# Optimization experiments

Hardware: AMD Instinct MI355X
Metric: run time of the kernel (lower is better)

The kernel has to match this reference:

```python
import jax, jax.numpy as jnp
import numpy as np

B, T, C, H = 4, 2048, 1024, 16
HD = C // H


def setup_inputs() -> dict:
    key = jax.random.key(0)
    kx, kq, ko = jax.random.split(key, 3)
    x = jax.random.normal(kx, (B, T, C), dtype=jnp.float32)
    # torch nn.Linear weight layout: [out_features, in_features]
    wqkv = jax.random.normal(kq, (3 * C, C), dtype=jnp.float32) * (1.0 / np.sqrt(C))
    wo = jax.random.normal(ko, (C, C), dtype=jnp.float32) * (1.0 / np.sqrt(C))
    return {"x": x, "wqkv": wqkv, "wo": wo}


def reference(x, wqkv, wo):
    Bn, Tn, Cn = x.shape
    # fused QKV projection: x @ wqkv.T -> [B, T, 3C]
    qkv = jnp.einsum('btc,dc->btd', x, wqkv)
    qkv = qkv.reshape(Bn, Tn, 3, H, HD)
    q = qkv[:, :, 0].transpose(0, 2, 1, 3)  # [B, H, T, hd]
    k = qkv[:, :, 1].transpose(0, 2, 1, 3)
    v = qkv[:, :, 2].transpose(0, 2, 1, 3)
    scale = 1.0 / np.sqrt(HD).astype(np.float32)
    scores = jnp.einsum('bhqd,bhkd->bhqk', q, k) * scale  # [B, H, T, T]
    causal = jnp.tril(jnp.ones((Tn, Tn), dtype=bool))
    scores = jnp.where(causal, scores, jnp.finfo(scores.dtype).min)
    attn = jax.nn.softmax(scores, axis=-1)
    y = jnp.einsum('bhqk,bhkd->bhqd', attn, v)  # [B, H, T, hd]
    y = y.transpose(0, 2, 1, 3).reshape(Bn, Tn, Cn)
    return jnp.einsum('btc,dc->btd', y, wo)
```

## Files before the change

### kernel.cpp

```cpp
#include <hip/hip_runtime.h>
#include <hip/hip_bf16.h>
#include <stdint.h>


typedef __attribute__((ext_vector_type(8))) short short8;
typedef __attribute__((ext_vector_type(4))) float f32x4;
typedef __attribute__((ext_vector_type(4))) float float4v;
typedef __attribute__((ext_vector_type(4))) unsigned short ushort4v;
typedef __attribute__((ext_vector_type(4))) unsigned int u32x4;

#define AS1 __attribute__((address_space(1)))
#define AS3 __attribute__((address_space(3)))

#if __has_builtin(__builtin_amdgcn_exp2f)
#define EXP2(x) __builtin_amdgcn_exp2f(x)
#else
#define EXP2(x) __expf((x) * 0.69314718f)
#endif

static __device__ __forceinline__ void gload_lds16(const void* g, void* l) {
  __builtin_amdgcn_global_load_lds((const AS1 void*)g, (AS3 void*)l, 16, 0, 0);
}

__global__ void k_detect(const unsigned int* __restrict__ x, int* __restrict__ flag) {
  __shared__ int sm[256];
  int c = 0;
  for (int i = 0; i < 8; ++i) {
    unsigned int v = x[threadIdx.x * 8 + i];
    unsigned int e = (v >> 7) & 0xffu;
    if (e >= 110u && e <= 140u) c++;
  }
  sm[threadIdx.x] = c;
  __syncthreads();
  if (threadIdx.x == 0) {
    int t = 0;
    for (int i = 0; i < 256; ++i) t += sm[i];
    *flag = (t > 1024) ? 1 : 0;
  }
}

__global__ void k_convert3(const void* __restrict__ xs, const void* __restrict__ wqs,
                           const void* __restrict__ wos, unsigned short* __restrict__ out,
                           const int* __restrict__ flag) {
  const int f = *flag;
  const int stride = gridDim.x * blockDim.x;
  for (int v = blockIdx.x * blockDim.x + threadIdx.x; v < 3145728; v += stride) {
    const int i = v * 4;
    const void* src; int j;
    if (i < 8388608)        { src = xs;  j = i; }
    else if (i < 11534336)  { src = wqs; j = i - 8388608; }
    else                    { src = wos; j = i - 11534336; }
    ushort4v r;
    if (f) {
      r = *(const ushort4v*)((const unsigned short*)src + j);
    } else {
      float4v fv = *(const float4v*)((const float*)src + j);
#pragma unroll
      for (int e = 0; e < 4; e++) {
        __hip_bfloat16 h = __float2bfloat16(fv[e]);
        r[e] = *(unsigned short*)&h;
      }
    }
    *(ushort4v*)(out + i) = r;
  }
}

__global__ __launch_bounds__(512) void k_gemm_qkv(
    const __hip_bfloat16* __restrict__ X, const __hip_bfloat16* __restrict__ W,
    __hip_bfloat16* __restrict__ qo, __hip_bfloat16* __restrict__ ko,
    __hip_bfloat16* __restrict__ vto) {
  __shared__ __align__(16) __hip_bfloat16 As[3][128 * 32];
  __shared__ __align__(16) __hip_bfloat16 Bs[3][128 * 32];
  const int tid = threadIdx.x;
  const int lane = tid & 63;
  const int wid = tid >> 6;
  const int wr = wid & 3, wc = wid >> 2;
  const int lr = lane & 15, lk = lane >> 4;
  const int m0 = blockIdx.x * 128;
  const int n0 = blockIdx.y * 128;
  const int sw = (lr >> 1) & 3;

  const int row = tid >> 2;
  const int ce = ((tid & 3) ^ ((row >> 1) & 3)) * 8;
  const int dst = (tid & ~63) * 8;

  const f32x4 fzero = {0.f, 0.f, 0.f, 0.f};
  f32x4 acc[2][4];
#pragma unroll
  for (int i = 0; i < 2; i++)
#pragma unroll
    for (int j = 0; j < 4; j++) acc[i][j] = fzero;

#define QKV_STAGE(buf, kt2)                                                        \
  {                                                                                \
    const int kk = (kt2) * 32;                                                     \
    gload_lds16(X + (size_t)(m0 + row) * 1024 + kk + ce, (void*)(As[buf] + dst));  \
    gload_lds16(W + (size_t)(n0 + row) * 1024 + kk + ce, (void*)(Bs[buf] + dst));  \
  }

  QKV_STAGE(0, 0)
  QKV_STAGE(1, 1)

  int cur = 0;
  for (int kt = 0; kt < 32; ++kt) {
    if (kt + 1 < 32) { asm volatile("s_waitcnt vmcnt(2)" ::: "memory"); }
    else             { asm volatile("s_waitcnt vmcnt(0)" ::: "memory"); }
    __builtin_amdgcn_s_barrier();
    __builtin_amdgcn_sched_barrier(0);

    short8 a[2], b[4];
#pragma unroll
    for (int i = 0; i < 2; i++) a[i] = *(const short8*)(As[cur] + (wr * 32 + i * 16 + lr) * 32 + ((lk ^ sw) * 8));
#pragma unroll
    for (int i = 0; i < 4; i++) b[i] = *(const short8*)(Bs[cur] + (wc * 64 + i * 16 + lr) * 32 + ((lk ^ sw) * 8));
#pragma unroll
    for (int mf = 0; mf < 2; mf++)
#pragma unroll
      for (int nf = 0; nf < 4; nf++)
        acc[mf][nf] = __builtin_amdgcn_mfma_f32_16x16x32_bf16(a[mf], b[nf], acc[mf][nf], 0, 0, 0);

    if (kt + 2 < 32) {
      int tb = cur + 2; if (tb >= 3) tb -= 3;
      QKV_STAGE(tb, kt + 2)
    }
    cur = (cur + 1 == 3) ? 0 : cur + 1;
  }
#undef QKV_STAGE

#pragma unroll
  for (int mf = 0; mf < 2; mf++)
#pragma unroll
    for (int nf = 0; nf < 4; nf++)
#pragma unroll
      for (int r = 0; r < 4; r++) {
        const int orow = m0 + wr * 32 + mf * 16 + lk * 4 + r;
        const int col = n0 + wc * 64 + nf * 16 + lr;
        const int s = col >> 10;
        const int rem = col & 1023;
        const int h = rem >> 6, hd = rem & 63;
        const int bb = orow >> 11, t = orow & 2047;
        const size_t bh = (size_t)(bb * 16 + h);
        if (s == 0) {
          qo[(bh * 2048 + t) * 64 + hd] = __float2bfloat16(acc[mf][nf][r] * 0.18033688f);
        } else if (s == 1) {
          ko[(bh * 2048 + t) * 64 + hd] = __float2bfloat16(acc[mf][nf][r]);
        } else {
          vto[(bh * 64 + hd) * 2048 + t] = __float2bfloat16(acc[mf][nf][r]);
        }
      }
}

__global__ __launch_bounds__(512) void k_attn(
    const __hip_bfloat16* __restrict__ Q, const __hip_bfloat16* __restrict__ K,
    const __hip_bfloat16* __restrict__ VT, __hip_bfloat16* __restrict__ Y) {
  __shared__ __align__(16) char smem[49152];
  char* smc = smem;
  const int tid = threadIdx.x, lane = tid & 63, wid = tid >> 6;
  const int lr = lane & 15, lk = lane >> 4;

  const int bid = blockIdx.x;
  const int bh = bid & 63;
  const int p = bid >> 6;
  const int e = p & 3;
  const int x = (p < 4) ? p : 7 - e;
  const int q0 = x * 256;
  const int qb = q0 + wid * 32;
  const size_t base = (size_t)bh * 2048 * 64;

  const int srow = tid >> 3;
  const int fs = (srow & 7) ^ ((2 * (srow >> 3)) & 7);
  const int scol = ((tid & 7) ^ fs) * 8;
  const __hip_bfloat16* kg = K + base + scol;
  const __hip_bfloat16* vg = VT + base + (size_t)srow * 2048 + scol;
  const int ldst = (tid & ~63) * 16;

  int koff[4][2], voff[4][2], kla[4];
#pragma unroll
  for (int a = 0; a < 4; a++) {
    const int ra = (lr >> 2) * 8 + (a & 1) * 4 + (lr & 3) + (a >> 1) * 32;
    const int fr = (ra & 7) ^ ((2 * (ra >> 3)) & 7);
    kla[a] = lk * 8 + (a & 1) * 4 + (a >> 1) * 32;
#pragma unroll
    for (int ks = 0; ks < 2; ks++)
      koff[a][ks] = ra * 128 + (((ks * 4 + lk) ^ fr) * 16);
  }
#pragma unroll
  for (int df = 0; df < 4; df++) {
    const int rv = df * 16 + lr;
    const int fv = (rv & 7) ^ ((2 * (rv >> 3)) & 7);
#pragma unroll
    for (int ks = 0; ks < 2; ks++)
      voff[df][ks] = rv * 128 + (((ks * 4 + lk) ^ fv) * 16);
  }

  short8 qf[2][2];
#pragma unroll
  for (int qg = 0; qg < 2; qg++)
#pragma unroll
    for (int ks = 0; ks < 2; ks++)
      qf[qg][ks] = *(const short8*)(Q + base + (size_t)(qb + qg * 16 + lr) * 64 + ks * 32 + lk * 8);

  const f32x4 fzero = {0.f, 0.f, 0.f, 0.f};
  f32x4 ot[2][4];
  float mrow[2] = {-1e30f, -1e30f}, lrow[2] = {0.f, 0.f};
#pragma unroll
  for (int qg = 0; qg < 2; qg++)
#pragma unroll
    for (int df = 0; df < 4; df++) ot[qg][df] = fzero;

  const int nkv = x * 4 + 4;
  gload_lds16(kg + (size_t)srow * 64, (void*)(smc + ldst));
  gload_lds16(vg, (void*)(smc + 24576 + ldst));
  gload_lds16(kg + (size_t)(64 + srow) * 64, (void*)(smc + 8192 + ldst));
  gload_lds16(vg + 64, (void*)(smc + 24576 + 8192 + ldst));

  int cur = 0;
  for (int kt = 0; kt < nkv; ++kt) {
    const int k0 = kt * 64;
    if (kt + 1 < nkv) { asm volatile("s_waitcnt vmcnt(2)" ::: "memory"); }
    else              { asm volatile("s_waitcnt vmcnt(0)" ::: "memory"); }
    __builtin_amdgcn_s_barrier();
    __builtin_amdgcn_sched_barrier(0);

    if (k0 <= qb + 31) {
      const char* kbuf = smc + cur * 8192;
      const char* vbuf = smc + 24576 + cur * 8192;

      f32x4 s[2][4];
#pragma unroll
      for (int qg = 0; qg < 2; qg++)
#pragma unroll
        for (int a = 0; a < 4; a++) s[qg][a] = fzero;

      __builtin_amdgcn_s_setprio(1);
#pragma unroll
      for (int ks = 0; ks < 2; ks++)
#pragma unroll
        for (int a = 0; a < 4; a++) {
          const short8 kb = *(const short8*)(kbuf + koff[a][ks]);
          s[0][a] = __builtin_amdgcn_mfma_f32_16x16x32_bf16(kb, qf[0][ks], s[0][a], 0, 0, 0);
          s[1][a] = __builtin_amdgcn_mfma_f32_16x16x32_bf16(kb, qf[1][ks], s[1][a], 0, 0, 0);
        }
      __builtin_amdgcn_s_setprio(0);

      const bool needmask = (k0 + 63 > qb);
      short8 pb[2][2];

#pragma unroll
      for (int qg = 0; qg < 2; qg++) {
        const int qq = qb + qg * 16 + lr;
        if (needmask) {
#pragma unroll
          for (int a = 0; a < 4; a++)
#pragma unroll
            for (int r = 0; r < 4; r++)
              if (k0 + kla[a] + r > qq) s[qg][a][r] = -1e30f;
        }
        f32x4 m4;
#pragma unroll
        for (int r = 0; r < 4; r++)
          m4[r] = fmaxf(fmaxf(s[qg][0][r], s[qg][1][r]), fmaxf(s[qg][2][r], s[qg][3][r]));
        float mx = fmaxf(fmaxf(m4[0], m4[1]), fmaxf(m4[2], m4[3]));
        mx = fmaxf(mx, __shfl_xor(mx, 16, 64));
        mx = fmaxf(mx, __shfl_xor(mx, 32, 64));
        const float mold = mrow[qg];
        float m;
        if (__all(mx - mold <= 8.f)) {
          m = mold;
        } else {
          m = fmaxf(mold, mx);
          const float alpha = EXP2(mold - m);
          lrow[qg] *= alpha;
          mrow[qg] = m;
#pragma unroll
          for (int df = 0; df < 4; df++) ot[qg][df] *= alpha;
        }
        float rs = 0.f;
#pragma unroll
        for (int a = 0; a < 4; a++)
#pragma unroll
          for (int r = 0; r < 4; r++) {
            const float pv = EXP2(s[qg][a][r] - m);
            s[qg][a][r] = pv;
            rs += pv;
          }
        lrow[qg] += rs;
#pragma unroll
        for (int ksP = 0; ksP < 2; ksP++) {
          short8 w;
#pragma unroll
          for (int ee = 0; ee < 4; ee++) {
            __hip_bfloat16 h0 = __float2bfloat16(s[qg][2 * ksP][ee]);
            __hip_bfloat16 h1 = __float2bfloat16(s[qg][2 * ksP + 1][ee]);
            w[ee] = *(short*)&h0;
            w[4 + ee] = *(short*)&h1;
          }
          pb[qg][ksP] = w;
        }
      }

      __builtin_amdgcn_s_setprio(1);
#pragma unroll
      for (int ks = 0; ks < 2; ks++)
#pragma unroll
        for (int df = 0; df < 4; df++) {
          const short8 vb = *(const short8*)(vbuf + voff[df][ks]);
          ot[0][df] = __builtin_amdgcn_mfma_f32_16x16x32_bf16(vb, pb[0][ks], ot[0][df], 0, 0, 0);
          ot[1][df] = __builtin_amdgcn_mfma_f32_16x16x32_bf16(vb, pb[1][ks], ot[1][df], 0, 0, 0);
        }
      __builtin_amdgcn_s_setprio(0);
    }

    if (kt + 2 < nkv) {
      const int kn = (kt + 2) * 64;
      int tb = cur + 2; if (tb >= 3) tb -= 3;
      gload_lds16(kg + (size_t)(kn + srow) * 64, (void*)(smc + tb * 8192 + ldst));
      gload_lds16(vg + kn, (void*)(smc + 24576 + tb * 8192 + ldst));
    }
    cur = (cur + 1 == 3) ? 0 : cur + 1;
  }

  __syncthreads();
  unsigned int* Os = (unsigned int*)smc;
#pragma unroll
  for (int qg = 0; qg < 2; qg++) {
    float ls = lrow[qg];
    ls += __shfl_xor(ls, 16, 64);
    ls += __shfl_xor(ls, 32, 64);
    const float inv = 1.f / ls;
    const int qlocal = wid * 32 + qg * 16 + lr;
    const int sw = (lr & 7) << 2;
#pragma unroll
    for (int df = 0; df < 4; df++)
#pragma unroll
      for (int e2 = 0; e2 < 2; e2++) {
        __hip_bfloat16 h0 = __float2bfloat16(ot[qg][df][2 * e2] * inv);
        __hip_bfloat16 h1 = __float2bfloat16(ot[qg][df][2 * e2 + 1] * inv);
        const unsigned int w = (unsigned int)*(unsigned short*)&h0 |
                               ((unsigned int)*(unsigned short*)&h1 << 16);
        Os[qlocal * 32 + ((df * 8 + lk * 2 + e2) ^ sw)] = w;
      }
  }
  __syncthreads();
  {
    const int qrow = tid >> 1, half = tid & 1, q7 = qrow & 7;
    const int b = bh >> 4, h = bh & 15;
    unsigned int* Yu = (unsigned int*)Y;
    const size_t rowbase = ((size_t)b * 2048 + q0 + qrow) * 512 + h * 32;
#pragma unroll
    for (int g = 0; g < 4; g++) {
      const int cg = half * 4 + g;
      const u32x4 v = *(const u32x4*)(smc + qrow * 128 + ((cg ^ q7) * 16));
      *(u32x4*)(Yu + rowbase + cg * 4) = v;
    }
  }
}

__global__ __launch_bounds__(512) void k_gemm_out(
    const __hip_bfloat16* __restrict__ X, const __hip_bfloat16* __restrict__ W,
    void* __restrict__ out, const int* __restrict__ flag) {
  __shared__ __align__(16) __hip_bfloat16 As[3][128 * 32];
  __shared__ __align__(16) __hip_bfloat16 Bs[3][128 * 32];
  const int tid = threadIdx.x;
  const int lane = tid & 63;
  const int wid = tid >> 6;
  const int wr = wid & 3, wc = wid >> 2;
  const int lr = lane & 15, lk = lane >> 4;
  const int m0 = blockIdx.x * 128;
  const int n0 = blockIdx.y * 128;
  const int sw = (lr >> 1) & 3;

  const int row = tid >> 2;
  const int ce = ((tid & 3) ^ ((row >> 1) & 3)) * 8;
  const int dst = (tid & ~63) * 8;

  const f32x4 fzero = {0.f, 0.f, 0.f, 0.f};
  f32x4 acc[2][4];
#pragma unroll
  for (int i = 0; i < 2; i++)
#pragma unroll
    for (int j = 0; j < 4; j++) acc[i][j] = fzero;

#define OUT_STAGE(buf, kt2)                                                        \
  {                                                                                \
    const int kk = (kt2) * 32;                                                     \
    gload_lds16(X + (size_t)(m0 + row) * 1024 + kk + ce, (void*)(As[buf] + dst));  \
    gload_lds16(W + (size_t)(n0 + row) * 1024 + kk + ce, (void*)(Bs[buf] + dst));  \
  }

  OUT_STAGE(0, 0)
  OUT_STAGE(1, 1)

  int cur = 0;
  for (int kt = 0; kt < 32; ++kt) {
    if (kt + 1 < 32) { asm volatile("s_waitcnt vmcnt(2)" ::: "memory"); }
    else             { asm volatile("s_waitcnt vmcnt(0)" ::: "memory"); }
    __builtin_amdgcn_s_barrier();
    __builtin_amdgcn_sched_barrier(0);

    short8 a[2], b[4];
#pragma unroll
    for (int i = 0; i < 2; i++) a[i] = *(const short8*)(As[cur] + (wr * 32 + i * 16 + lr) * 32 + ((lk ^ sw) * 8));
#pragma unroll
    for (int i = 0; i < 4; i++) b[i] = *(const short8*)(Bs[cur] + (wc * 64 + i * 16 + lr) * 32 + ((lk ^ sw) * 8));
#pragma unroll
    for (int mf = 0; mf < 2; mf++)
#pragma unroll
      for (int nf = 0; nf < 4; nf++)
        acc[mf][nf] = __builtin_amdgcn_mfma_f32_16x16x32_bf16(a[mf], b[nf], acc[mf][nf], 0, 0, 0);

    if (kt + 2 < 32) {
      int tb = cur + 2; if (tb >= 3) tb -= 3;
      OUT_STAGE(tb, kt + 2)
    }
    cur = (cur + 1 == 3) ? 0 : cur + 1;
  }
#undef OUT_STAGE

  const int f = *flag;
#pragma unroll
  for (int mf = 0; mf < 2; mf++)
#pragma unroll
    for (int nf = 0; nf < 4; nf++)
#pragma unroll
      for (int r = 0; r < 4; r++) {
        const int orow = m0 + wr * 32 + mf * 16 + lk * 4 + r;
        const int col = n0 + wc * 64 + nf * 16 + lr;
        const size_t oi = (size_t)orow * 1024 + col;
        if (f) ((__hip_bfloat16*)out)[oi] = __float2bfloat16(acc[mf][nf][r]);
        else   ((float*)out)[oi] = acc[mf][nf][r];
      }
}

extern "C" void kernel_launch(void* const* d_in, const int* in_sizes, int n_in,
                              void* d_out, int out_size, void* d_ws, size_t ws_size,
                              hipStream_t stream) {
  const void* x = d_in[0];
  const void* wqkv = d_in[1];
  const void* wo = d_in[2];

  char* ws = (char*)d_ws;
  int* flag = (int*)ws;
  __hip_bfloat16* xb    = (__hip_bfloat16*)(ws + 256);
  __hip_bfloat16* wqkvb = xb + 8388608;
  __hip_bfloat16* wob   = wqkvb + 3145728;
  __hip_bfloat16* qws   = wob + 1048576;
  __hip_bfloat16* kws   = qws + 8388608;
  __hip_bfloat16* vtws  = kws + 8388608;
  __hip_bfloat16* yws   = xb;

  k_detect<<<1, 256, 0, stream>>>((const unsigned int*)x, flag);
  k_convert3<<<2048, 256, 0, stream>>>(x, wqkv, wo, (unsigned short*)xb, flag);

  dim3 g1(64, 24);
  k_gemm_qkv<<<g1, 512, 0, stream>>>(xb, wqkvb, qws, kws, vtws);

  k_attn<<<512, 512, 0, stream>>>(qws, kws, vtws, yws);

  dim3 g3(64, 8);
  k_gemm_out<<<g3, 512, 0, stream>>>(yws, wob, d_out, flag);
}
```

Baseline: 180.7 us.

## Enlarge QKV GEMM tiles to 256x256x64 with swizzled block mapping

Measured after the change: 227.9 us. 26.1% more time.

```diff
diff --git a/kernel.cpp b/kernel.cpp
--- a/kernel.cpp
+++ b/kernel.cpp
@@ -69,83 +69,108 @@
     const __hip_bfloat16* __restrict__ X, const __hip_bfloat16* __restrict__ W,
     __hip_bfloat16* __restrict__ qo, __hip_bfloat16* __restrict__ ko,
     __hip_bfloat16* __restrict__ vto) {
-  __shared__ __align__(16) __hip_bfloat16 As[3][128 * 32];
-  __shared__ __align__(16) __hip_bfloat16 Bs[3][128 * 32];
+  __shared__ __align__(16) __hip_bfloat16 As[2][256 * 64];
+  __shared__ __align__(16) __hip_bfloat16 Bs[2][256 * 64];
   const int tid = threadIdx.x;
   const int lane = tid & 63;
   const int wid = tid >> 6;
-  const int wr = wid & 3, wc = wid >> 2;
+  const int wm = wid & 1, wn = wid >> 1;
   const int lr = lane & 15, lk = lane >> 4;
-  const int m0 = blockIdx.x * 128;
-  const int n0 = blockIdx.y * 128;
-  const int sw = (lr >> 1) & 3;
-
-  const int row = tid >> 2;
-  const int ce = ((tid & 3) ^ ((row >> 1) & 3)) * 8;
-  const int dst = (tid & ~63) * 8;
+
+  const int bid = blockIdx.x;
+  const int swz = (bid & 7) * 48 + (bid >> 3);
+  const int m0 = (swz & 31) * 256;
+  const int n0 = (swz >> 5) * 256;
+
+  const int srow = tid >> 3;
+  const int schunk = ((tid & 7) ^ (srow & 7)) * 8;
+  const int sdst = (tid & ~63) * 16;
+
+  int aoff[2], boff[2];
+#pragma unroll
+  for (int ks = 0; ks < 2; ks++) {
+    const int px = (((ks * 4 + lk) ^ (lr & 7)) * 16);
+    aoff[ks] = (wm * 128 + lr) * 128 + px;
+    boff[ks] = (wn * 64 + lr) * 128 + px;
+  }
 
   const f32x4 fzero = {0.f, 0.f, 0.f, 0.f};
-  f32x4 acc[2][4];
-#pragma unroll
-  for (int i = 0; i < 2; i++)
+  f32x4 acc[8][4];
+#pragma unroll
+  for (int i = 0; i < 8; i++)
 #pragma unroll
     for (int j = 0; j < 4; j++) acc[i][j] = fzero;
 
-#define QKV_STAGE(buf, kt2)                                                        \
-  {                                                                                \
-    const int kk = (kt2) * 32;                                                     \
-    gload_lds16(X + (size_t)(m0 + row) * 1024 + kk + ce, (void*)(As[buf] + dst));  \
-    gload_lds16(W + (size_t)(n0 + row) * 1024 + kk + ce, (void*)(Bs[buf] + dst));  \
-  }
-
-  QKV_STAGE(0, 0)
-  QKV_STAGE(1, 1)
-
-  int cur = 0;
-  for (int kt = 0; kt < 32; ++kt) {
-    if (kt + 1 < 32) { asm volatile("s_waitcnt vmcnt(2)" ::: "memory"); }
-    else             { asm volatile("s_waitcnt vmcnt(0)" ::: "memory"); }
+#define QSTG(buf, kt2, j)                                                           \
+  gload_lds16(X + (size_t)(m0 + (j) * 64 + srow) * 1024 + (kt2) * 64 + schunk,      \
+              (void*)((char*)As + (buf) * 32768 + (j) * 8192 + sdst));              \
+  gload_lds16(W + (size_t)(n0 + (j) * 64 + srow) * 1024 + (kt2) * 64 + schunk,      \
+              (void*)((char*)Bs + (buf) * 32768 + (j) * 8192 + sdst));
+
+  QSTG(0, 0, 0) QSTG(0, 0, 1) QSTG(0, 0, 2) QSTG(0, 0, 3)
+
+  for (int kt = 0; kt < 16; ++kt) {
+    asm volatile("s_waitcnt vmcnt(0)" ::: "memory");
     __builtin_amdgcn_s_barrier();
     __builtin_amdgcn_sched_barrier(0);
-
-    short8 a[2], b[4];
-#pragma unroll
-    for (int i = 0; i < 2; i++) a[i] = *(const short8*)(As[cur] + (wr * 32 + i * 16 + lr) * 32 + ((lk ^ sw) * 8));
-#pragma unroll
-    for (int i = 0; i < 4; i++) b[i] = *(const short8*)(Bs[cur] + (wc * 64 + i * 16 + lr) * 32 + ((lk ^ sw) * 8));
-#pragma unroll
-    for (int mf = 0; mf < 2; mf++)
-#pragma unroll
-      for (int nf = 0; nf < 4; nf++)
-        acc[mf][nf] = __builtin_amdgcn_mfma_f32_16x16x32_bf16(a[mf], b[nf], acc[mf][nf], 0, 0, 0);
-
-    if (kt + 2 < 32) {
-      int tb = cur + 2; if (tb >= 3) tb -= 3;
-      QKV_STAGE(tb, kt + 2)
-    }
-    cur = (cur + 1 == 3) ? 0 : cur + 1;
-  }
-#undef QKV_STAGE
-
-#pragma unroll
-  for (int mf = 0; mf < 2; mf++)
-#pragma unroll
-    for (int nf = 0; nf < 4; nf++)
+    const int buf = kt & 1;
+    const int nb = buf ^ 1;
+    const char* Ab = (const char*)As + buf * 32768;
+    const char* Bb = (const char*)Bs + buf * 32768;
+
+    short8 bf[4][2];
+#pragma unroll
+    for (int q = 0; q < 4; ++q) {
+      if (q == 0 && kt + 1 < 16) { QSTG(nb, kt + 1, 0) QSTG(nb, kt + 1, 1) }
+      if (q == 1 && kt + 1 < 16) { QSTG(nb, kt + 1, 2) QSTG(nb, kt + 1, 3) }
+      if (q == 0) {
+#pragma unroll
+        for (int fc = 0; fc < 4; fc++)
+#pragma unroll
+          for (int ks = 0; ks < 2; ks++)
+            bf[fc][ks] = *(const short8*)(Bb + fc * 2048 + boff[ks]);
+      }
+      short8 af[2][2];
+#pragma unroll
+      for (int i = 0; i < 2; i++)
+#pragma unroll
+        for (int ks = 0; ks < 2; ks++)
+          af[i][ks] = *(const short8*)(Ab + (2 * q + i) * 2048 + aoff[ks]);
+      asm volatile("s_waitcnt lgkmcnt(0)" ::: "memory");
+      __builtin_amdgcn_sched_barrier(0);
+      __builtin_amdgcn_s_setprio(1);
+#pragma unroll
+      for (int ks = 0; ks < 2; ks++)
+#pragma unroll
+        for (int i = 0; i < 2; i++)
+#pragma unroll
+          for (int fc = 0; fc < 4; fc++)
+            acc[2 * q + i][fc] = __builtin_amdgcn_mfma_f32_16x16x32_bf16(
+                af[i][ks], bf[fc][ks], acc[2 * q + i][fc], 0, 0, 0);
+      __builtin_amdgcn_s_setprio(0);
+    }
+  }
+#undef QSTG
+
+#pragma unroll
+  for (int fr = 0; fr < 8; fr++)
+#pragma unroll
+    for (int fc = 0; fc < 4; fc++)
 #pragma unroll
       for (int r = 0; r < 4; r++) {
-        const int orow = m0 + wr * 32 + mf * 16 + lk * 4 + r;
-        const int col = n0 + wc * 64 + nf * 16 + lr;
+        const int orow = m0 + wm * 128 + fr * 16 + lk * 4 + r;
+        const int col = n0 + wn * 64 + fc * 16 + lr;
         const int s = col >> 10;
         const int rem = col & 1023;
         const int h = rem >> 6, hd = rem & 63;
         const int bb = orow >> 11, t = orow & 2047;
         const size_t bh = (size_t)(bb * 16 + h);
         if (s == 0) {
-          qo[(bh * 2048 + t) * 64 + hd] = __float2bfloat16(acc[mf][nf][r] * 0.18033688f);
+          qo[(bh * 2048 + t) * 64 + hd] = __float2bfloat16(acc[fr][fc][r] * 0.18033688f);
         } else if (s == 1) {
-          ko[(bh * 2048 + t) * 64 + hd] = __float2bfloat16(acc[mf][nf][r]);
+          ko[(bh * 2048 + t) * 64 + hd] = __float2bfloat16(acc[fr][fc][r]);
         } else {
-          vto[(bh * 64 + hd) * 2048 + t] = __float2bfloat16(acc[mf][nf][r]);
+          vto[(bh * 64 + hd) * 2048 + t] = __float2bfloat16(acc[fr][fc][r]);
         }
       }
 }
@@ -452,8 +477,7 @@
   k_detect<<<1, 256, 0, stream>>>((const unsigned int*)x, flag);
   k_convert3<<<2048, 256, 0, stream>>>(x, wqkv, wo, (unsigned short*)xb, flag);
 
-  dim3 g1(64, 24);
-  k_gemm_qkv<<<g1, 512, 0, stream>>>(xb, wqkvb, qws, kws, vtws);
+  k_gemm_qkv<<<384, 512, 0, stream>>>(xb, wqkvb, qws, kws, vtws);
 
   k_attn<<<512, 512, 0, stream>>>(qws, kws, vtws, yws);
 
```
